# Kernel optimization log

Hardware: AMD Instinct MI355X
Metric: run time of the kernel (lower is better)

Reference implementation:

```python
import jax, jax.numpy as jnp
import numpy as np

N_SEQ, L, DH, DX, M, G, N_TOK, N_MEM, N_TYP = 1024, 64, 256, 128, 8192, 4096, 10000, 262144, 64

def setup_inputs() -> dict:
    key = jax.random.key(0)
    ks = jax.random.split(key, 16)
    s_q = 1.0 / np.sqrt(2 * DH)
    s_k = 1.0 / np.sqrt(DH)
    s_r = 1.0 / np.sqrt(2 * DH + DX)
    msk = jax.random.randint(ks[4], (N_SEQ, L), 0, 2).astype(jnp.int32)
    msk = msk.at[:, 0].set(1)  # guarantee >=1 valid position per sequence
    return {
        "mem": jax.random.randint(ks[0], (N_MEM,), 0, N_TOK),
        "grp": jax.random.randint(ks[1], (N_MEM,), 0, G),
        "pos2grp": jax.random.randint(ks[2], (N_SEQ, L), 0, G),
        "h_grp": jax.random.normal(ks[3], (N_SEQ, L, DH), jnp.float32),
        "msk": msk,
        "idx": jnp.sort(jax.random.randint(ks[5], (M,), 0, N_SEQ)),
        "src": jax.random.randint(ks[6], (M,), 0, L),
        "dst": jax.random.randint(ks[7], (M,), 0, L),
        "typ": jax.random.randint(ks[8], (M, N_TYP), 0, 2).astype(jnp.int32),
        "tok_emb": jax.random.normal(ks[9], (N_TOK, DX), jnp.float32),
        "Wq": jax.random.normal(ks[10], (2 * DH, DH), jnp.float32) * s_q,
        "bq": jnp.zeros((DH,), jnp.float32),
        "Wk": jax.random.normal(ks[11], (DH, DH), jnp.float32) * s_k,
        "bk": jnp.zeros((DH,), jnp.float32),
        "Wrel": jax.random.normal(ks[12], (2 * DH + DX, N_TYP), jnp.float32) * s_r,
        "brel": jnp.zeros((N_TYP,), jnp.float32),
    }

def reference(mem, grp, pos2grp, h_grp, msk, idx, src, dst, typ,
              tok_emb, Wq, bq, Wk, bk, Wrel, brel):
    # z_grp = scatter_sum(tok_encoder(mem), grp, 0)[pos2grp]  -> (n, l, dx)
    z = jax.ops.segment_sum(tok_emb[mem], grp, num_segments=G)
    z_grp = z[pos2grp]
    # q = cat(h_grp[idx, src], h_grp[idx, dst])  -> (M, 2*dh)
    q = jnp.concatenate([h_grp[idx, src], h_grp[idx, dst]], axis=-1)
    qp = q @ Wq + bq                                    # (M, dh)
    kp = jnp.einsum('nld,de->nle', h_grp, Wk) + bk      # (n, l, dh)
    # repeat_interleave(nq) over sorted-by-group queries == gather by idx
    scores = jnp.einsum('mld,md->ml', kp[idx], qp) / jnp.sqrt(jnp.float32(DH))
    scores = jnp.where(msk[idx].astype(bool), scores, -jnp.inf)
    attn = jax.nn.softmax(scores, axis=1)               # (M, l)
    ctx = jnp.einsum('ml,mlv->mv', attn, z_grp[idx])    # (M, dx)
    logit = jnp.concatenate([q, ctx], axis=-1) @ Wrel + brel  # (M, n_typ)
    return logit
```

## Files before the change

kernel.cpp:

```cpp
#include <hip/hip_runtime.h>
#include <math.h>

#define N_SEQ 1024
#define LL 64
#define DH 256
#define DX 128
#define MQ 8192
#define GG 4096
#define NTYP 64
#define NMEM 262144

typedef __attribute__((ext_vector_type(8))) short short8v;
typedef __attribute__((ext_vector_type(4))) float float4v;

__device__ __forceinline__ unsigned short f2bf(float x) {
    unsigned int u = __float_as_uint(x);
    u += 0x7FFFu + ((u >> 16) & 1u);
    return (unsigned short)(u >> 16);
}

__global__ __launch_bounds__(256) void k_init(const float* __restrict__ Wq,
                                              unsigned short* __restrict__ WqB,
                                              int4* __restrict__ cnt4,
                                              const int* __restrict__ idx,
                                              int* __restrict__ ofs_n) {
    int b = blockIdx.x, tid = threadIdx.x;
    if (b < 128) {
        int i = (b * 256 + tid) * 4;
        float4 v = *(const float4*)(Wq + i);
        ushort4 o;
        o.x = f2bf(v.x); o.y = f2bf(v.y); o.z = f2bf(v.z); o.w = f2bf(v.w);
        *(ushort4*)(WqB + i) = o;
    } else if (b < 132) {
        cnt4[(b - 128) * 256 + tid] = (int4){0, 0, 0, 0};
    } else {
        int n = (b - 132) * 256 + tid;
        int lo = 0, hi = MQ;
        while (lo < hi) {
            int mid = (lo + hi) >> 1;
            if (idx[mid] < n) lo = mid + 1; else hi = mid;
        }
        ofs_n[n] = lo;
        if (n == 0) ofs_n[N_SEQ] = MQ;
    }
}

__global__ __launch_bounds__(256) void k_histw(const int* __restrict__ grp,
                                               int* __restrict__ cnt,
                                               int* __restrict__ rank,
                                               const float* __restrict__ Wk,
                                               const float* __restrict__ bq,
                                               const unsigned short* __restrict__ WqB,
                                               const float* __restrict__ Wrel,
                                               const float* __restrict__ brel,
                                               unsigned short* __restrict__ BT,
                                               float* __restrict__ bias) {
    __shared__ __align__(16) unsigned short A[16 * 256];
    __shared__ float bred[16][17];
    int b = blockIdx.x, tid = threadIdx.x;
    if (b < 1024) {
        int i = b * 256 + tid;
        rank[i] = atomicAdd(&cnt[grp[i]], 1);
        return;
    }
    int b2 = b - 1024;
    if (b2 < 16) {
        int n0 = b2 * 16;
        {
            int r = tid >> 4;
            int kc = (tid & 15) * 16;
            const float4* s4 = (const float4*)(Wk + (size_t)(n0 + r) * 256 + kc);
            unsigned short* Arow = A + r * 256;
#pragma unroll
            for (int j = 0; j < 2; ++j) {
                float4 lo = s4[j * 2], hi = s4[j * 2 + 1];
                unsigned short tmp[8];
                tmp[0] = f2bf(lo.x); tmp[1] = f2bf(lo.y);
                tmp[2] = f2bf(lo.z); tmp[3] = f2bf(lo.w);
                tmp[4] = f2bf(hi.x); tmp[5] = f2bf(hi.y);
                tmp[6] = f2bf(hi.z); tmp[7] = f2bf(hi.w);
                int c = (kc >> 3) + j;
                int cs = (c & ~7) | ((c & 7) ^ (r & 7));
                *(int4*)(Arow + cs * 8) = *(int4*)tmp;
            }
        }
        __syncthreads();
        int w = tid >> 6, lane = tid & 63;
        int r = lane & 15, kq = lane >> 4;
        float4v acc[8];
#pragma unroll
        for (int t = 0; t < 8; ++t) acc[t] = (float4v){0.f, 0.f, 0.f, 0.f};
        const unsigned short* Arow = A + r * 256;
#pragma unroll
        for (int ks = 0; ks < 8; ++ks) {
            int c = ks * 4 + kq;
            int cs = (c & ~7) | ((c & 7) ^ (r & 7));
            short8v a = *(const short8v*)(Arow + cs * 8);
            int kk = ks * 32 + kq * 8;
#pragma unroll
            for (int t = 0; t < 8; ++t) {
                int jcol = w * 128 + t * 16 + r;
                short8v bf = *(const short8v*)(WqB + (size_t)jcol * 256 + kk);
                acc[t] = __builtin_amdgcn_mfma_f32_16x16x32_bf16(a, bf, acc[t], 0, 0, 0);
            }
        }
#pragma unroll
        for (int t = 0; t < 8; ++t) {
            int jcol = w * 128 + t * 16 + r;
#pragma unroll
            for (int j = 0; j < 4; ++j)
                BT[(size_t)(n0 + kq * 4 + j) * 512 + jcol] = f2bf(acc[t][j]);
        }
        {
            int n16 = tid >> 4, seg = tid & 15;
            const float* wkr = Wk + (size_t)(n0 + n16) * 256 + seg * 16;
            const float* bqr = bq + seg * 16;
            float pb = 0.f;
#pragma unroll
            for (int i = 0; i < 16; ++i) pb += wkr[i] * bqr[i];
            bred[n16][seg] = pb;
        }
        __syncthreads();
        if (tid < 16) {
            float s = 0.f;
#pragma unroll
            for (int k2 = 0; k2 < 16; ++k2) s += bred[tid][k2];
            bias[n0 + tid] = s;
        }
    } else {
        int t0 = (b2 - 16) * 16;
#pragma unroll
        for (int jj = 0; jj < 2; ++jj) {
            int j = tid + jj * 256;
            const float* wr = Wrel + (size_t)j * NTYP + t0;
#pragma unroll
            for (int tt = 0; tt < 16; ++tt)
                BT[(size_t)(256 + t0 + tt) * 512 + j] = f2bf(wr[tt]);
        }
        if (b2 == 16 && tid < 64) bias[256 + tid] = brel[tid];
    }
}

__global__ __launch_bounds__(1024) void k_scan(const int* __restrict__ cnt,
                                               int* __restrict__ ofs) {
    __shared__ int wsum[16];
    int tid = threadIdx.x;
    int4 c = ((const int4*)cnt)[tid];
    int local = c.x + c.y + c.z + c.w;
    int lane = tid & 63, w = tid >> 6;
    int v = local;
    for (int off = 1; off < 64; off <<= 1) {
        int t = __shfl_up(v, off);
        if (lane >= off) v += t;
    }
    if (lane == 63) wsum[w] = v;
    __syncthreads();
    if (tid < 16) {
        int s = wsum[tid];
        for (int off = 1; off < 16; off <<= 1) {
            int t = __shfl_up(s, off);
            if (tid >= off) s += t;
        }
        wsum[tid] = s;
    }
    __syncthreads();
    int base = (w > 0 ? wsum[w - 1] : 0) + (v - local);
    int4 o;
    o.x = base;
    o.y = base + c.x;
    o.z = o.y + c.y;
    o.w = o.z + c.z;
    ((int4*)ofs)[tid] = o;
}

__global__ __launch_bounds__(256) void k_pg(const int* __restrict__ grp,
                                            const int* __restrict__ mem,
                                            const int* __restrict__ ofs,
                                            const int* __restrict__ rank,
                                            int* __restrict__ tok_sorted,
                                            const float* __restrict__ h_grp,
                                            const int* __restrict__ idx,
                                            const int* __restrict__ srcv,
                                            const int* __restrict__ dstv,
                                            const unsigned short* __restrict__ BT,
                                            const float* __restrict__ bias,
                                            unsigned short* __restrict__ qkb,
                                            float* __restrict__ part) {
    __shared__ __align__(16) unsigned short A[16 * 512];
    __shared__ int ns[16], ss[16], dsv[16];
    int b = blockIdx.x, tid = threadIdx.x;
    if (b < 1024) {
        int i = b * 256 + tid;
        tok_sorted[ofs[grp[i]] + rank[i]] = mem[i];
        return;
    }
    int bid = b - 1024;
    int swz = (bid & 7) * 64 + (bid >> 3);
    int m0 = swz * 16;
    if (tid < 16) {
        int m = m0 + tid;
        ns[tid] = idx[m];
        ss[tid] = srcv[m];
        dsv[tid] = dstv[m];
    }
    __syncthreads();
    {
        int r = tid >> 4;
        int kc = (tid & 15) * 32;
        const float* src = h_grp +
            ((size_t)ns[r] * LL + (kc < 256 ? ss[r] : dsv[r])) * DH + (kc & 255);
        const float4* s4 = (const float4*)src;
        float4 f[8];
#pragma unroll
        for (int j = 0; j < 8; ++j) f[j] = s4[j];
        unsigned short* Arow = A + r * 512;
#pragma unroll
        for (int j = 0; j < 4; ++j) {
            int c = (kc >> 3) + j;
            int cs = (c & ~7) | ((c & 7) ^ (r & 7));
            unsigned short tmp[8];
            float4 lo = f[j * 2], hi = f[j * 2 + 1];
            tmp[0] = f2bf(lo.x); tmp[1] = f2bf(lo.y);
            tmp[2] = f2bf(lo.z); tmp[3] = f2bf(lo.w);
            tmp[4] = f2bf(hi.x); tmp[5] = f2bf(hi.y);
            tmp[6] = f2bf(hi.z); tmp[7] = f2bf(hi.w);
            *(int4*)(Arow + cs * 8) = *(int4*)tmp;
        }
    }
    __syncthreads();

    int w = tid >> 6, lane = tid & 63;
    int r = lane & 15;
    int q = lane >> 4;
    int n0 = w * 80;
    float4v acc[5];
#pragma unroll
    for (int t = 0; t < 5; ++t) {
        float b3 = bias[n0 + t * 16 + r];
        acc[t] = (float4v){b3, b3, b3, b3};
    }
    const unsigned short* Arow = A + r * 512;
#pragma unroll 2
    for (int ks = 0; ks < 16; ++ks) {
        int c = ks * 4 + q;
        int cs = (c & ~7) | ((c & 7) ^ (r & 7));
        short8v a = *(const short8v*)(Arow + cs * 8);
        int kk = ks * 32 + q * 8;
#pragma unroll
        for (int t = 0; t < 5; ++t) {
            int n = n0 + t * 16 + r;
            short8v b3 = *(const short8v*)(BT + (size_t)n * 512 + kk);
            acc[t] = __builtin_amdgcn_mfma_f32_16x16x32_bf16(a, b3, acc[t], 0, 0, 0);
        }
    }
#pragma unroll
    for (int t = 0; t < 5; ++t) {
        int n = n0 + t * 16 + r;
        if (n < 256) {
#pragma unroll
            for (int j = 0; j < 4; ++j)
                qkb[(size_t)(m0 + q * 4 + j) * 256 + n] = f2bf(acc[t][j]);
        } else {
#pragma unroll
            for (int j = 0; j < 4; ++j)
                part[(size_t)(m0 + q * 4 + j) * NTYP + (n - 256)] = acc[t][j];
        }
    }
}

__global__ __launch_bounds__(128) void k_zsum(const int* __restrict__ ofs,
                                              const int* __restrict__ cnt,
                                              const int* __restrict__ tok_sorted,
                                              const float* __restrict__ tok_emb,
                                              const float* __restrict__ Wrel,
                                              float* __restrict__ zw) {
    __shared__ int idxs[128];
    __shared__ float red[4][128];
    __shared__ float zs[128];
    int g = blockIdx.x;
    int tid = threadIdx.x;
    int gq = tid >> 5;
    int s = tid & 31;
    int start = ofs[g], n = cnt[g];
    float4 a0 = {0.f, 0.f, 0.f, 0.f}, a1 = {0.f, 0.f, 0.f, 0.f};
    for (int j0 = 0; j0 < n; j0 += 128) {
        __syncthreads();
        int rem = n - j0;
        if (tid < rem) idxs[tid] = tok_sorted[start + j0 + tid];
        __syncthreads();
        int kmax = rem < 128 ? rem : 128;
        int k = gq;
        for (; k + 4 < kmax; k += 8) {
            const float4* r0 = (const float4*)(tok_emb + (size_t)idxs[k] * DX);
            const float4* r1 = (const float4*)(tok_emb + (size_t)idxs[k + 4] * DX);
            float4 v0 = r0[s], v1 = r1[s];
            a0.x += v0.x; a0.y += v0.y; a0.z += v0.z; a0.w += v0.w;
            a1.x += v1.x; a1.y += v1.y; a1.z += v1.z; a1.w += v1.w;
        }
        if (k < kmax) {
            const float4* r0 = (const float4*)(tok_emb + (size_t)idxs[k] * DX);
            float4 v0 = r0[s];
            a0.x += v0.x; a0.y += v0.y; a0.z += v0.z; a0.w += v0.w;
        }
    }
    a0.x += a1.x; a0.y += a1.y; a0.z += a1.z; a0.w += a1.w;
    ((float4*)red[gq])[s] = a0;
    __syncthreads();
    zs[tid] = red[0][tid] + red[1][tid] + red[2][tid] + red[3][tid];
    __syncthreads();
    if (tid < NTYP) {
        float a2s = 0.f;
#pragma unroll 8
        for (int v = 0; v < DX; ++v)
            a2s += zs[v] * Wrel[(size_t)(512 + v) * NTYP + tid];
        zw[(size_t)g * NTYP + tid] = a2s;
    }
}

__global__ __launch_bounds__(256) void k_attn9(const float* __restrict__ h_grp,
                                               const int* __restrict__ ofs_n,
                                               const int* __restrict__ pos2grp,
                                               const int* __restrict__ msk,
                                               const float* __restrict__ zw,
                                               const unsigned short* __restrict__ qkb,
                                               const float* __restrict__ part,
                                               float* __restrict__ out) {
    __shared__ __align__(16) unsigned short zwT[64][72];
    __shared__ __align__(16) unsigned short PsT[16][72];
    __shared__ float red0[4][16], red1[4][16];

    int bid = blockIdx.x;
    int n = (bid & 7) * 128 + (bid >> 3);
    int start = ofs_n[n];
    int nq = ofs_n[n + 1] - start;
    if (nq <= 0) return;

    int tid = threadIdx.x;
    int w = tid >> 6, lane = tid & 63;
    int q15 = lane & 15, kq = lane >> 4;

    int mk = msk[n * LL + lane];
    int gv = pos2grp[n * LL + lane];

    {
        int l = 16 * w + (lane >> 2);
        int cb = (lane & 3) * 16;
        int gl = __shfl(gv, l);
        const float4* zr4 = (const float4*)(zw + (size_t)gl * NTYP + cb);
#pragma unroll
        for (int i4 = 0; i4 < 4; ++i4) {
            float4 zv = zr4[i4];
            zwT[cb + i4 * 4 + 0][l] = f2bf(zv.x);
            zwT[cb + i4 * 4 + 1][l] = f2bf(zv.y);
            zwT[cb + i4 * 4 + 2][l] = f2bf(zv.z);
            zwT[cb + i4 * 4 + 3][l] = f2bf(zv.w);
        }
    }

    const float* hrow = h_grp + ((size_t)n * LL + 16 * w + q15) * DH;
    short8v afrag[8];
#pragma unroll
    for (int ks = 0; ks < 8; ++ks) {
        const float4* p = (const float4*)(hrow + ks * 32 + kq * 8);
        float4 f0 = p[0], f1 = p[1];
        unsigned short t[8];
        t[0] = f2bf(f0.x); t[1] = f2bf(f0.y);
        t[2] = f2bf(f0.z); t[3] = f2bf(f0.w);
        t[4] = f2bf(f1.x); t[5] = f2bf(f1.y);
        t[6] = f2bf(f1.z); t[7] = f2bf(f1.w);
        afrag[ks] = *(short8v*)t;
    }
    __syncthreads();

    for (int t0 = 0; t0 < nq; t0 += 16) {
        int nqt = nq - t0; if (nqt > 16) nqt = 16;
        if (t0 > 0) __syncthreads();

        int mq = start + t0 + (q15 < nqt ? q15 : 0);
        const unsigned short* qrow = qkb + (size_t)mq * 256;
        float4v sacc = (float4v){0.f, 0.f, 0.f, 0.f};
#pragma unroll
        for (int ks = 0; ks < 8; ++ks) {
            short8v b = *(const short8v*)(qrow + ks * 32 + kq * 8);
            sacc = __builtin_amdgcn_mfma_f32_16x16x32_bf16(afrag[ks], b, sacc, 0, 0, 0);
        }
        float sv[4];
#pragma unroll
        for (int j = 0; j < 4; ++j) {
            int l = 16 * w + kq * 4 + j;
            int mkl = __shfl(mk, l);
            sv[j] = mkl ? sacc[j] * 0.0625f : -INFINITY;
        }
        float pmax = fmaxf(fmaxf(sv[0], sv[1]), fmaxf(sv[2], sv[3]));
        pmax = fmaxf(pmax, __shfl_xor(pmax, 16));
        pmax = fmaxf(pmax, __shfl_xor(pmax, 32));
        if (lane < 16) red0[w][lane] = pmax;
        __syncthreads();
        float mx = fmaxf(fmaxf(red0[0][q15], red0[1][q15]),
                         fmaxf(red0[2][q15], red0[3][q15]));
        float pe[4];
        float psum = 0.f;
#pragma unroll
        for (int j = 0; j < 4; ++j) { pe[j] = __expf(sv[j] - mx); psum += pe[j]; }
        psum += __shfl_xor(psum, 16);
        psum += __shfl_xor(psum, 32);
        if (lane < 16) red1[w][lane] = psum;
        __syncthreads();
        float inv = 1.0f / (red1[0][q15] + red1[1][q15] + red1[2][q15] + red1[3][q15]);
        ushort4 pk;
        pk.x = f2bf(pe[0] * inv); pk.y = f2bf(pe[1] * inv);
        pk.z = f2bf(pe[2] * inv); pk.w = f2bf(pe[3] * inv);
        *(ushort4*)(&PsT[q15][16 * w + kq * 4]) = pk;
        __syncthreads();

        float4v cacc[4];
#pragma unroll
        for (int ct = 0; ct < 4; ++ct) cacc[ct] = (float4v){0.f, 0.f, 0.f, 0.f};
#pragma unroll
        for (int ks = 0; ks < 2; ++ks) {
            short8v a = *(const short8v*)(&PsT[q15][ks * 32 + kq * 8]);
#pragma unroll
            for (int ct = 0; ct < 4; ++ct) {
                short8v b = *(const short8v*)(&zwT[ct * 16 + q15][ks * 32 + kq * 8]);
                cacc[ct] = __builtin_amdgcn_mfma_f32_16x16x32_bf16(a, b, cacc[ct], 0, 0, 0);
            }
        }
#pragma unroll
        for (int ct = 0; ct < 4; ++ct) {
            int col = ct * 16 + q15;
#pragma unroll
            for (int j = 0; j < 4; ++j) {
                int qrow2 = kq * 4 + j;
                if (qrow2 < nqt) {
                    size_t m = (size_t)(start + t0 + qrow2);
                    out[m * NTYP + col] = part[m * NTYP + col] + cacc[ct][j];
                }
            }
        }
    }
}

extern "C" void kernel_launch(void* const* d_in, const int* in_sizes, int n_in,
                              void* d_out, int out_size, void* d_ws, size_t ws_size,
                              hipStream_t stream) {
    const int*   mem     = (const int*)d_in[0];
    const int*   grp     = (const int*)d_in[1];
    const int*   pos2grp = (const int*)d_in[2];
    const float* h_grp   = (const float*)d_in[3];
    const int*   msk     = (const int*)d_in[4];
    const int*   idx     = (const int*)d_in[5];
    const int*   srcv    = (const int*)d_in[6];
    const int*   dstv    = (const int*)d_in[7];
    const float* tok_emb = (const float*)d_in[9];
    const float* Wq      = (const float*)d_in[10];
    const float* bq      = (const float*)d_in[11];
    const float* Wk      = (const float*)d_in[12];
    const float* bk      = (const float*)d_in[13];
    const float* Wrel    = (const float*)d_in[14];
    const float* brel    = (const float*)d_in[15];
    float* out = (float*)d_out;
    (void)bk;

    float* ws = (float*)d_ws;
    size_t off = 0;
    float* zw   = ws + off; off += (size_t)GG * NTYP;
    unsigned short* qkb = (unsigned short*)(ws + off); off += (size_t)MQ * 256 / 2;
    float* part = ws + off; off += (size_t)MQ * NTYP;
    float* bias = ws + off; off += 320;
    unsigned short* BT  = (unsigned short*)(ws + off); off += (320 * 512) / 2;
    unsigned short* WqB = (unsigned short*)(ws + off); off += (512 * 256) / 2;
    int* cnt        = (int*)(ws + off); off += GG;
    int* ofs        = (int*)(ws + off); off += GG;
    int* rank       = (int*)(ws + off); off += NMEM;
    int* tok_sorted = (int*)(ws + off); off += NMEM;
    int* ofs_n      = (int*)(ws + off); off += N_SEQ + 1;

    k_init<<<136, 256, 0, stream>>>(Wq, WqB, (int4*)cnt, idx, ofs_n);

    k_histw<<<1044, 256, 0, stream>>>(grp, cnt, rank, Wk, bq, WqB, Wrel, brel,
                                      BT, bias);

    k_scan<<<1, 1024, 0, stream>>>(cnt, ofs);

    k_pg<<<1536, 256, 0, stream>>>(grp, mem, ofs, rank, tok_sorted,
                                   h_grp, idx, srcv, dstv, BT, bias, qkb, part);

    k_zsum<<<GG, 128, 0, stream>>>(ofs, cnt, tok_sorted, tok_emb, Wrel, zw);

    k_attn9<<<N_SEQ, 256, 0, stream>>>(h_grp, ofs_n, pos2grp, msk, zw, qkb, part, out);
}
```

Before: 111.0 us.

## Fold prefix scan into projection GEMM kernel and split permute into its own launch

The single-block scan kernel is removed. Block 0 of the projection GEMM kernel now computes the exclusive prefix over group counts, with 16 counts per thread across 256 threads. The token permutation, which needs those offsets, moves to a separate kernel launched afterwards. Launch count stays the same, but the serial scan now overlaps with the GEMM blocks instead of standing alone on the critical path. The trade-off is that the permutation can no longer share a launch with the GEMM work.

```diff
diff --git a/kernel.cpp b/kernel.cpp
--- a/kernel.cpp
+++ b/kernel.cpp
@@ -141,43 +141,8 @@
     }
 }
 
-__global__ __launch_bounds__(1024) void k_scan(const int* __restrict__ cnt,
-                                               int* __restrict__ ofs) {
-    __shared__ int wsum[16];
-    int tid = threadIdx.x;
-    int4 c = ((const int4*)cnt)[tid];
-    int local = c.x + c.y + c.z + c.w;
-    int lane = tid & 63, w = tid >> 6;
-    int v = local;
-    for (int off = 1; off < 64; off <<= 1) {
-        int t = __shfl_up(v, off);
-        if (lane >= off) v += t;
-    }
-    if (lane == 63) wsum[w] = v;
-    __syncthreads();
-    if (tid < 16) {
-        int s = wsum[tid];
-        for (int off = 1; off < 16; off <<= 1) {
-            int t = __shfl_up(s, off);
-            if (tid >= off) s += t;
-        }
-        wsum[tid] = s;
-    }
-    __syncthreads();
-    int base = (w > 0 ? wsum[w - 1] : 0) + (v - local);
-    int4 o;
-    o.x = base;
-    o.y = base + c.x;
-    o.z = o.y + c.y;
-    o.w = o.z + c.z;
-    ((int4*)ofs)[tid] = o;
-}
-
-__global__ __launch_bounds__(256) void k_pg(const int* __restrict__ grp,
-                                            const int* __restrict__ mem,
-                                            const int* __restrict__ ofs,
-                                            const int* __restrict__ rank,
-                                            int* __restrict__ tok_sorted,
+__global__ __launch_bounds__(256) void k_sg(const int* __restrict__ cnt,
+                                            int* __restrict__ ofs,
                                             const float* __restrict__ h_grp,
                                             const int* __restrict__ idx,
                                             const int* __restrict__ srcv,
@@ -189,12 +154,30 @@
     __shared__ __align__(16) unsigned short A[16 * 512];
     __shared__ int ns[16], ss[16], dsv[16];
     int b = blockIdx.x, tid = threadIdx.x;
-    if (b < 1024) {
-        int i = b * 256 + tid;
-        tok_sorted[ofs[grp[i]] + rank[i]] = mem[i];
+    if (b == 0) {
+        int* wsum = (int*)A;
+        int lane = tid & 63, w = tid >> 6;
+        int c[16];
+        int tsum = 0;
+        int base0 = tid * 16;
+#pragma unroll
+        for (int j = 0; j < 16; ++j) { c[j] = cnt[base0 + j]; tsum += c[j]; }
+        int v = tsum;
+        for (int o2 = 1; o2 < 64; o2 <<= 1) {
+            int t = __shfl_up(v, o2);
+            if (lane >= o2) v += t;
+        }
+        if (lane == 63) wsum[w] = v;
+        __syncthreads();
+        int wb = 0;
+#pragma unroll
+        for (int q2 = 0; q2 < 4; ++q2) if (q2 < w) wb += wsum[q2];
+        int base = wb + v - tsum;
+#pragma unroll
+        for (int j = 0; j < 16; ++j) { ofs[base0 + j] = base; base += c[j]; }
         return;
     }
-    int bid = b - 1024;
+    int bid = b - 1;
     int swz = (bid & 7) * 64 + (bid >> 3);
     int m0 = swz * 16;
     if (tid < 16) {
@@ -266,6 +249,15 @@
                 part[(size_t)(m0 + q * 4 + j) * NTYP + (n - 256)] = acc[t][j];
         }
     }
+}
+
+__global__ __launch_bounds__(256) void k_permute(const int* __restrict__ grp,
+                                                 const int* __restrict__ mem,
+                                                 const int* __restrict__ ofs,
+                                                 const int* __restrict__ rank,
+                                                 int* __restrict__ tok_sorted) {
+    int i = blockIdx.x * 256 + threadIdx.x;
+    if (i < NMEM) tok_sorted[ofs[grp[i]] + rank[i]] = mem[i];
 }
 
 __global__ __launch_bounds__(128) void k_zsum(const int* __restrict__ ofs,
@@ -480,10 +472,10 @@
     k_histw<<<1044, 256, 0, stream>>>(grp, cnt, rank, Wk, bq, WqB, Wrel, brel,
                                       BT, bias);
 
-    k_scan<<<1, 1024, 0, stream>>>(cnt, ofs);
-
-    k_pg<<<1536, 256, 0, stream>>>(grp, mem, ofs, rank, tok_sorted,
-                                   h_grp, idx, srcv, dstv, BT, bias, qkb, part);
+    k_sg<<<513, 256, 0, stream>>>(cnt, ofs, h_grp, idx, srcv, dstv, BT, bias,
+                                  qkb, part);
+
+    k_permute<<<NMEM / 256, 256, 0, stream>>>(grp, mem, ofs, rank, tok_sorted);
 
     k_zsum<<<GG, 128, 0, stream>>>(ofs, cnt, tok_sorted, tok_emb, Wrel, zw);
 
```

After: 102.1 us. -8.1%, faster.
